# Performance work log

Hardware: AMD Instinct MI355X
Metric: run time of the kernel (lower is better)

Reference implementation:

```python
import jax, jax.numpy as jnp
import numpy as np

B, T, I = 8192, 20, 16
H1, H2, FC = 128, 64, 32


def _lstm(x_tbi, Wih, Whh, bih, bhh, H):
    """PyTorch-convention LSTM. x_tbi: (T,B,in). Gate order: i,f,g,o. Returns (T,B,H) hidden seq."""
    Tn, Bn = x_tbi.shape[0], x_tbi.shape[1]
    # precompute input projection for all timesteps: (T,B,4H)
    xz = jnp.einsum('tbi,gi->tbg', x_tbi, Wih) + (bih + bhh)

    def step(carry, xz_t):
        h, c = carry
        z = xz_t + h @ Whh.T  # (B,4H)
        i = jax.nn.sigmoid(z[:, 0*H:1*H])
        f = jax.nn.sigmoid(z[:, 1*H:2*H])
        g = jnp.tanh(z[:, 2*H:3*H])
        o = jax.nn.sigmoid(z[:, 3*H:4*H])
        c = f * c + i * g
        h = o * jnp.tanh(c)
        return (h, c), h

    h0 = jnp.zeros((Bn, H), x_tbi.dtype)
    c0 = jnp.zeros((Bn, H), x_tbi.dtype)
    _, hs = jax.lax.scan(step, (h0, c0), xz)
    return hs  # (T,B,H)


def setup_inputs() -> dict:
    key = jax.random.key(0)
    ks = jax.random.split(key, 16)
    s1 = 1.0 / np.sqrt(H1)
    s2 = 1.0 / np.sqrt(H2)
    u = lambda k, shape, s: jax.random.uniform(k, shape, jnp.float32, -s, s)
    return {
        'x': jax.random.normal(ks[0], (B, T, I), jnp.float32),
        'Wih1': u(ks[1], (4 * H1, I), s1),
        'Whh1': u(ks[2], (4 * H1, H1), s1),
        'bih1': u(ks[3], (4 * H1,), s1),
        'bhh1': u(ks[4], (4 * H1,), s1),
        'Wih2': u(ks[5], (4 * H2, H1), s2),
        'Whh2': u(ks[6], (4 * H2, H2), s2),
        'bih2': u(ks[7], (4 * H2,), s2),
        'bhh2': u(ks[8], (4 * H2,), s2),
        'gamma': jnp.ones((H2,), jnp.float32),
        'beta': jnp.zeros((H2,), jnp.float32),
        'W1': u(ks[9], (FC, H2), 1.0 / np.sqrt(H2)),
        'b1': u(ks[10], (FC,), 1.0 / np.sqrt(H2)),
        'W2': u(ks[11], (1, FC), 1.0 / np.sqrt(FC)),
        'b2': u(ks[12], (1,), 1.0 / np.sqrt(FC)),
    }


def reference(x, Wih1, Whh1, bih1, bhh1, Wih2, Whh2, bih2, bhh2, gamma, beta, W1, b1, W2, b2):
    # dropout layers are identity (eval mode)
    x_tbi = jnp.transpose(x, (1, 0, 2))           # (T,B,I)
    out1 = _lstm(x_tbi, Wih1, Whh1, bih1, bhh1, H1)  # (T,B,H1)
    out2 = _lstm(out1, Wih2, Whh2, bih2, bhh2, H2)   # (T,B,H2)
    last = out2[-1]                               # (B,H2)
    # LayerNorm over H2
    mu = jnp.mean(last, axis=-1, keepdims=True)
    var = jnp.mean((last - mu) ** 2, axis=-1, keepdims=True)
    normed = (last - mu) * jax.lax.rsqrt(var + 1e-5) * gamma + beta
    h = jax.nn.relu(normed @ W1.T + b1)           # (B,FC)
    logit = h @ W2.T + b2                         # (B,1)
    return logit[:, 0]
```

## Files before the change

kernel.cpp:

```cpp
#include <hip/hip_runtime.h>

#define TS 20
#define BATCH 8192
#define LOG2E 1.4426950408889634f

typedef _Float16 half8 __attribute__((ext_vector_type(8)));
typedef float f32x4 __attribute__((ext_vector_type(4)));

__device__ __forceinline__ float fexp2(float x) {
#if __has_builtin(__builtin_amdgcn_exp2f)
    return __builtin_amdgcn_exp2f(x);
#else
    return exp2f(x);
#endif
}
__device__ __forceinline__ float sig2(float zp)  { return __builtin_amdgcn_rcpf(1.0f + fexp2(-zp)); }
__device__ __forceinline__ float tanh2(float zp) { return 1.0f - 2.0f * __builtin_amdgcn_rcpf(1.0f + fexp2(zp)); }
__device__ __forceinline__ int swz(int r) { return (r & 7) ^ (((r >> 3) & 1) << 2); }

extern "C" __global__ __launch_bounds__(512, 1)
void fused_lstm_kernel(const float* __restrict__ x,
                       const float* __restrict__ Wih1, const float* __restrict__ Whh1,
                       const float* __restrict__ bih1, const float* __restrict__ bhh1,
                       const float* __restrict__ Wih2, const float* __restrict__ Whh2,
                       const float* __restrict__ bih2, const float* __restrict__ bhh2,
                       const float* __restrict__ gamma, const float* __restrict__ beta,
                       const float* __restrict__ W1fc, const float* __restrict__ b1fc,
                       const float* __restrict__ W2fc, const float* __restrict__ b2fc,
                       float* __restrict__ out)
{
    __shared__ __align__(16) _Float16 bf2l[4 * 4 * 6 * 64 * 8];
    __shared__ __align__(16) _Float16 Hb[2][2][16][128];
    __shared__ __align__(16) _Float16 Hc[2][2][16][72];
    __shared__ __align__(16) _Float16 Xb[32][328];
    __shared__ float h2f[32][68];

    const int tid  = threadIdx.x;
    const int lane = tid & 63;
    const int w    = tid >> 6;
    const int lrow = lane & 15;
    const int lgrp = lane >> 4;
    const int b0   = blockIdx.x * 32;

    half8 bf[4][5];
    float bias1[4];
#pragma unroll
    for (int g = 0; g < 4; ++g) {
        const float sc = (g == 2) ? 2.0f * LOG2E : LOG2E;
        const int n = g * 128 + w * 16 + lrow;
        bias1[g] = (bih1[n] + bhh1[n]) * sc;
#pragma unroll
        for (int ch = 0; ch < 5; ++ch) {
            half8 v;
            if (ch < 4) {
                const float4 p0 = *(const float4*)&Whh1[n * 128 + ch * 32 + lgrp * 8];
                const float4 p1 = *(const float4*)&Whh1[n * 128 + ch * 32 + lgrp * 8 + 4];
                v[0]=(_Float16)(p0.x*sc); v[1]=(_Float16)(p0.y*sc); v[2]=(_Float16)(p0.z*sc); v[3]=(_Float16)(p0.w*sc);
                v[4]=(_Float16)(p1.x*sc); v[5]=(_Float16)(p1.y*sc); v[6]=(_Float16)(p1.z*sc); v[7]=(_Float16)(p1.w*sc);
            } else if (lgrp < 2) {
                const float4 p0 = *(const float4*)&Wih1[n * 16 + lgrp * 8];
                const float4 p1 = *(const float4*)&Wih1[n * 16 + lgrp * 8 + 4];
                v[0]=(_Float16)(p0.x*sc); v[1]=(_Float16)(p0.y*sc); v[2]=(_Float16)(p0.z*sc); v[3]=(_Float16)(p0.w*sc);
                v[4]=(_Float16)(p1.x*sc); v[5]=(_Float16)(p1.y*sc); v[6]=(_Float16)(p1.z*sc); v[7]=(_Float16)(p1.w*sc);
            } else {
#pragma unroll
                for (int j = 0; j < 8; ++j) v[j] = (_Float16)0.0f;
            }
            bf[g][ch] = v;
        }
    }

    const int cg = w & 3;
    const int mt = w >> 2;
    float bias2[4];
#pragma unroll
    for (int g = 0; g < 4; ++g) {
        const float sc = (g == 2) ? 2.0f * LOG2E : LOG2E;
        const int n = g * 64 + cg * 16 + lrow;
        bias2[g] = (bih2[n] + bhh2[n]) * sc;
    }
    if (w < 4) {
#pragma unroll
        for (int g = 0; g < 4; ++g) {
            const float sc = (g == 2) ? 2.0f * LOG2E : LOG2E;
            const int n = g * 64 + w * 16 + lrow;
#pragma unroll
            for (int ch = 0; ch < 6; ++ch) {
                const float4 p0 = (ch < 4) ? *(const float4*)&Wih2[n * 128 + ch * 32 + lgrp * 8]
                                           : *(const float4*)&Whh2[n * 64 + (ch - 4) * 32 + lgrp * 8];
                const float4 p1 = (ch < 4) ? *(const float4*)&Wih2[n * 128 + ch * 32 + lgrp * 8 + 4]
                                           : *(const float4*)&Whh2[n * 64 + (ch - 4) * 32 + lgrp * 8 + 4];
                half8 v;
                v[0]=(_Float16)(p0.x*sc); v[1]=(_Float16)(p0.y*sc); v[2]=(_Float16)(p0.z*sc); v[3]=(_Float16)(p0.w*sc);
                v[4]=(_Float16)(p1.x*sc); v[5]=(_Float16)(p1.y*sc); v[6]=(_Float16)(p1.z*sc); v[7]=(_Float16)(p1.w*sc);
                ((half8*)bf2l)[((w * 4 + g) * 6 + ch) * 64 + lane] = v;
            }
        }
    }

    for (int i = tid; i < 2 * 2 * 16 * 128; i += 512) (&Hb[0][0][0][0])[i] = (_Float16)0.0f;
    for (int i = tid; i < 2 * 2 * 16 * 72;  i += 512) (&Hc[0][0][0][0])[i] = (_Float16)0.0f;
    for (int i = tid; i < 32 * 320; i += 512) {
        const int r = i / 320, k = i % 320;
        Xb[r][k] = (_Float16)x[(size_t)(b0 + r) * 320 + k];
    }
    half8 kzero;
#pragma unroll
    for (int j = 0; j < 8; ++j) kzero[j] = (_Float16)0.0f;

    float c1[2][4] = {{0.f,0.f,0.f,0.f},{0.f,0.f,0.f,0.f}};
    float c2[4] = {0.f, 0.f, 0.f, 0.f};
    const int hu  = (w << 1) | (lrow >> 3);
    const int hlo = lrow & 7;
    const int szr = swz(lrow);
    const int cell2 = (cg << 4) | lrow;

    __syncthreads();

    for (int t = 0; t < TS; ++t) {
        const int s = t & 1;
        f32x4 z[2][4];
#pragma unroll
        for (int tile = 0; tile < 2; ++tile)
#pragma unroll
            for (int g = 0; g < 4; ++g) z[tile][g] = (f32x4){bias1[g], bias1[g], bias1[g], bias1[g]};
#pragma unroll
        for (int ch = 0; ch < 5; ++ch) {
#pragma unroll
            for (int tile = 0; tile < 2; ++tile) {
                half8 a;
                if (ch < 4) a = *(const half8*)&Hb[s ^ 1][tile][lrow][(((ch << 2) | lgrp) ^ szr) * 8];
                else        a = (lgrp < 2) ? *(const half8*)&Xb[tile * 16 + lrow][t * 16 + lgrp * 8] : kzero;
#pragma unroll
                for (int g = 0; g < 4; ++g)
                    z[tile][g] = __builtin_amdgcn_mfma_f32_16x16x32_f16(a, bf[g][ch], z[tile][g], 0, 0, 0);
            }
        }
#pragma unroll
        for (int tile = 0; tile < 2; ++tile)
#pragma unroll
            for (int j = 0; j < 4; ++j) {
                const float iv = sig2 (z[tile][0][j]);
                const float fv = sig2 (z[tile][1][j]);
                const float gv = tanh2(z[tile][2][j]);
                const float ov = sig2 (z[tile][3][j]);
                const float cn = fv * c1[tile][j] + iv * gv;
                c1[tile][j] = cn;
                const float h = ov * tanh2(2.0f * LOG2E * cn);
                const int m = (lgrp << 2) | j;
                Hb[s][tile][m][((hu ^ swz(m)) << 3) | hlo] = (_Float16)h;
            }
        __syncthreads();
        {
            half8 a2[6];
#pragma unroll
            for (int ch = 0; ch < 4; ++ch)
                a2[ch] = *(const half8*)&Hb[s][mt][lrow][(((ch << 2) | lgrp) ^ szr) * 8];
#pragma unroll
            for (int ch = 4; ch < 6; ++ch)
                a2[ch] = *(const half8*)&Hc[s ^ 1][mt][lrow][(ch - 4) * 32 + lgrp * 8];
            f32x4 z2[4];
#pragma unroll
            for (int g = 0; g < 4; ++g) {
                f32x4 acc = {bias2[g], bias2[g], bias2[g], bias2[g]};
#pragma unroll
                for (int ch = 0; ch < 6; ++ch) {
                    const half8 bfrag = ((const half8*)bf2l)[((cg * 4 + g) * 6 + ch) * 64 + lane];
                    acc = __builtin_amdgcn_mfma_f32_16x16x32_f16(a2[ch], bfrag, acc, 0, 0, 0);
                }
                z2[g] = acc;
            }
#pragma unroll
            for (int j = 0; j < 4; ++j) {
                const float iv = sig2 (z2[0][j]);
                const float fv = sig2 (z2[1][j]);
                const float gv = tanh2(z2[2][j]);
                const float ov = sig2 (z2[3][j]);
                const float cn = fv * c2[j] + iv * gv;
                c2[j] = cn;
                const float h = ov * tanh2(2.0f * LOG2E * cn);
                const int m = (lgrp << 2) | j;
                Hc[s][mt][m][cell2] = (_Float16)h;
                if (t == TS - 1) h2f[(mt << 4) | m][cell2] = h;
            }
        }
    }
    __syncthreads();

    {
        const int m = tid >> 4, q = tid & 15;
        const float v0 = h2f[m][q * 4 + 0];
        const float v1 = h2f[m][q * 4 + 1];
        const float v2 = h2f[m][q * 4 + 2];
        const float v3 = h2f[m][q * 4 + 3];
        float ssum = v0 + v1 + v2 + v3;
        ssum += __shfl_xor(ssum, 1); ssum += __shfl_xor(ssum, 2);
        ssum += __shfl_xor(ssum, 4); ssum += __shfl_xor(ssum, 8);
        const float mean = ssum * (1.0f / 64.0f);
        const float d0 = v0 - mean, d1 = v1 - mean, d2 = v2 - mean, d3 = v3 - mean;
        float vs = d0 * d0 + d1 * d1 + d2 * d2 + d3 * d3;
        vs += __shfl_xor(vs, 1); vs += __shfl_xor(vs, 2);
        vs += __shfl_xor(vs, 4); vs += __shfl_xor(vs, 8);
        const float rstd = rsqrtf(vs * (1.0f / 64.0f) + 1e-5f);
        const int i0 = q * 4;
        h2f[m][i0 + 0] = d0 * rstd * gamma[i0 + 0] + beta[i0 + 0];
        h2f[m][i0 + 1] = d1 * rstd * gamma[i0 + 1] + beta[i0 + 1];
        h2f[m][i0 + 2] = d2 * rstd * gamma[i0 + 2] + beta[i0 + 2];
        h2f[m][i0 + 3] = d3 * rstd * gamma[i0 + 3] + beta[i0 + 3];
    }
    __syncthreads();
    {
        const int o = tid & 31;
        const int mgrp = tid >> 5;
#pragma unroll
        for (int rr = 0; rr < 2; ++rr) {
            const int m = mgrp + rr * 16;
            float acc = b1fc[o];
#pragma unroll 8
            for (int k = 0; k < 64; ++k) acc += h2f[m][k] * W1fc[o * 64 + k];
            const float hv = fmaxf(acc, 0.0f);
            float p = hv * W2fc[o];
            p += __shfl_xor(p, 1); p += __shfl_xor(p, 2);
            p += __shfl_xor(p, 4); p += __shfl_xor(p, 8); p += __shfl_xor(p, 16);
            if (o == 0) out[b0 + m] = p + b2fc[0];
        }
    }
}

extern "C" void kernel_launch(void* const* d_in, const int* in_sizes, int n_in,
                              void* d_out, int out_size, void* d_ws, size_t ws_size,
                              hipStream_t stream) {
    (void)in_sizes; (void)n_in; (void)d_ws; (void)ws_size; (void)out_size;
    const float* x_p    = (const float*)d_in[0];
    const float* Wih1_p = (const float*)d_in[1];
    const float* Whh1_p = (const float*)d_in[2];
    const float* bih1_p = (const float*)d_in[3];
    const float* bhh1_p = (const float*)d_in[4];
    const float* Wih2_p = (const float*)d_in[5];
    const float* Whh2_p = (const float*)d_in[6];
    const float* bih2_p = (const float*)d_in[7];
    const float* bhh2_p = (const float*)d_in[8];
    const float* gamma_p = (const float*)d_in[9];
    const float* beta_p  = (const float*)d_in[10];
    const float* W1_p   = (const float*)d_in[11];
    const float* b1_p   = (const float*)d_in[12];
    const float* W2_p   = (const float*)d_in[13];
    const float* b2_p   = (const float*)d_in[14];
    float* out_p = (float*)d_out;

    fused_lstm_kernel<<<dim3(BATCH / 32), dim3(512), 0, stream>>>(
        x_p, Wih1_p, Whh1_p, bih1_p, bhh1_p,
        Wih2_p, Whh2_p, bih2_p, bhh2_p,
        gamma_p, beta_p, W1_p, b1_p, W2_p, b2_p, out_p);
}
```

Measured before the change: 77.85 us.

## Halve block to 256 threads and skew layer-2 one step behind layer-1

The block shrinks from 8 to 4 waves. Each wave now computes two layer-1 column groups, keeping their weights in registers, and both batch tiles of layer 2. Layer 2 for step t-1 runs inside the same barrier interval as layer 1 for step t, with a final drain step after the loop, so one __syncthreads per timestep is removed. The aim is fewer barriers and possibly two blocks per CU given the relaxed launch bounds. In exchange each wave does twice the MFMA work per step and register pressure rises (40 half8 weight fragments), which may cut occupancy or cause spills.

```diff
diff --git a/kernel.cpp b/kernel.cpp
--- a/kernel.cpp
+++ b/kernel.cpp
@@ -18,16 +18,16 @@
 __device__ __forceinline__ float tanh2(float zp) { return 1.0f - 2.0f * __builtin_amdgcn_rcpf(1.0f + fexp2(zp)); }
 __device__ __forceinline__ int swz(int r) { return (r & 7) ^ (((r >> 3) & 1) << 2); }
 
-extern "C" __global__ __launch_bounds__(512, 1)
-void fused_lstm_kernel(const float* __restrict__ x,
-                       const float* __restrict__ Wih1, const float* __restrict__ Whh1,
-                       const float* __restrict__ bih1, const float* __restrict__ bhh1,
-                       const float* __restrict__ Wih2, const float* __restrict__ Whh2,
-                       const float* __restrict__ bih2, const float* __restrict__ bhh2,
-                       const float* __restrict__ gamma, const float* __restrict__ beta,
-                       const float* __restrict__ W1fc, const float* __restrict__ b1fc,
-                       const float* __restrict__ W2fc, const float* __restrict__ b2fc,
-                       float* __restrict__ out)
+extern "C" __global__ __launch_bounds__(256)
+void fused_lstm_fat_kernel(const float* __restrict__ x,
+                           const float* __restrict__ Wih1, const float* __restrict__ Whh1,
+                           const float* __restrict__ bih1, const float* __restrict__ bhh1,
+                           const float* __restrict__ Wih2, const float* __restrict__ Whh2,
+                           const float* __restrict__ bih2, const float* __restrict__ bhh2,
+                           const float* __restrict__ gamma, const float* __restrict__ beta,
+                           const float* __restrict__ W1fc, const float* __restrict__ b1fc,
+                           const float* __restrict__ W2fc, const float* __restrict__ b2fc,
+                           float* __restrict__ out)
 {
     __shared__ __align__(16) _Float16 bf2l[4 * 4 * 6 * 64 * 8];
     __shared__ __align__(16) _Float16 Hb[2][2][16][128];
@@ -42,65 +42,59 @@
     const int lgrp = lane >> 4;
     const int b0   = blockIdx.x * 32;
 
-    half8 bf[4][5];
-    float bias1[4];
+    half8 bf1[2][4][5];
+    float bias1[2][4];
+#pragma unroll
+    for (int cgi = 0; cgi < 2; ++cgi) {
+        const int cg = w + cgi * 4;
+#pragma unroll
+        for (int g = 0; g < 4; ++g) {
+            const float sc = (g == 2) ? 2.0f * LOG2E : LOG2E;
+            const int n = g * 128 + cg * 16 + lrow;
+            bias1[cgi][g] = (bih1[n] + bhh1[n]) * sc;
+#pragma unroll
+            for (int ch = 0; ch < 5; ++ch) {
+                half8 v;
+                if (ch < 4) {
+                    const float4 p0 = *(const float4*)&Whh1[n * 128 + ch * 32 + lgrp * 8];
+                    const float4 p1 = *(const float4*)&Whh1[n * 128 + ch * 32 + lgrp * 8 + 4];
+                    v[0]=(_Float16)(p0.x*sc); v[1]=(_Float16)(p0.y*sc); v[2]=(_Float16)(p0.z*sc); v[3]=(_Float16)(p0.w*sc);
+                    v[4]=(_Float16)(p1.x*sc); v[5]=(_Float16)(p1.y*sc); v[6]=(_Float16)(p1.z*sc); v[7]=(_Float16)(p1.w*sc);
+                } else if (lgrp < 2) {
+                    const float4 p0 = *(const float4*)&Wih1[n * 16 + lgrp * 8];
+                    const float4 p1 = *(const float4*)&Wih1[n * 16 + lgrp * 8 + 4];
+                    v[0]=(_Float16)(p0.x*sc); v[1]=(_Float16)(p0.y*sc); v[2]=(_Float16)(p0.z*sc); v[3]=(_Float16)(p0.w*sc);
+                    v[4]=(_Float16)(p1.x*sc); v[5]=(_Float16)(p1.y*sc); v[6]=(_Float16)(p1.z*sc); v[7]=(_Float16)(p1.w*sc);
+                } else {
+#pragma unroll
+                    for (int j = 0; j < 8; ++j) v[j] = (_Float16)0.0f;
+                }
+                bf1[cgi][g][ch] = v;
+            }
+        }
+    }
+    float bias2[4];
 #pragma unroll
     for (int g = 0; g < 4; ++g) {
         const float sc = (g == 2) ? 2.0f * LOG2E : LOG2E;
-        const int n = g * 128 + w * 16 + lrow;
-        bias1[g] = (bih1[n] + bhh1[n]) * sc;
-#pragma unroll
-        for (int ch = 0; ch < 5; ++ch) {
+        const int n = g * 64 + w * 16 + lrow;
+        bias2[g] = (bih2[n] + bhh2[n]) * sc;
+#pragma unroll
+        for (int ch = 0; ch < 6; ++ch) {
+            const float4 p0 = (ch < 4) ? *(const float4*)&Wih2[n * 128 + ch * 32 + lgrp * 8]
+                                       : *(const float4*)&Whh2[n * 64 + (ch - 4) * 32 + lgrp * 8];
+            const float4 p1 = (ch < 4) ? *(const float4*)&Wih2[n * 128 + ch * 32 + lgrp * 8 + 4]
+                                       : *(const float4*)&Whh2[n * 64 + (ch - 4) * 32 + lgrp * 8 + 4];
             half8 v;
-            if (ch < 4) {
-                const float4 p0 = *(const float4*)&Whh1[n * 128 + ch * 32 + lgrp * 8];
-                const float4 p1 = *(const float4*)&Whh1[n * 128 + ch * 32 + lgrp * 8 + 4];
-                v[0]=(_Float16)(p0.x*sc); v[1]=(_Float16)(p0.y*sc); v[2]=(_Float16)(p0.z*sc); v[3]=(_Float16)(p0.w*sc);
-                v[4]=(_Float16)(p1.x*sc); v[5]=(_Float16)(p1.y*sc); v[6]=(_Float16)(p1.z*sc); v[7]=(_Float16)(p1.w*sc);
-            } else if (lgrp < 2) {
-                const float4 p0 = *(const float4*)&Wih1[n * 16 + lgrp * 8];
-                const float4 p1 = *(const float4*)&Wih1[n * 16 + lgrp * 8 + 4];
-                v[0]=(_Float16)(p0.x*sc); v[1]=(_Float16)(p0.y*sc); v[2]=(_Float16)(p0.z*sc); v[3]=(_Float16)(p0.w*sc);
-                v[4]=(_Float16)(p1.x*sc); v[5]=(_Float16)(p1.y*sc); v[6]=(_Float16)(p1.z*sc); v[7]=(_Float16)(p1.w*sc);
-            } else {
-#pragma unroll
-                for (int j = 0; j < 8; ++j) v[j] = (_Float16)0.0f;
-            }
-            bf[g][ch] = v;
-        }
-    }
-
-    const int cg = w & 3;
-    const int mt = w >> 2;
-    float bias2[4];
-#pragma unroll
-    for (int g = 0; g < 4; ++g) {
-        const float sc = (g == 2) ? 2.0f * LOG2E : LOG2E;
-        const int n = g * 64 + cg * 16 + lrow;
-        bias2[g] = (bih2[n] + bhh2[n]) * sc;
-    }
-    if (w < 4) {
-#pragma unroll
-        for (int g = 0; g < 4; ++g) {
-            const float sc = (g == 2) ? 2.0f * LOG2E : LOG2E;
-            const int n = g * 64 + w * 16 + lrow;
-#pragma unroll
-            for (int ch = 0; ch < 6; ++ch) {
-                const float4 p0 = (ch < 4) ? *(const float4*)&Wih2[n * 128 + ch * 32 + lgrp * 8]
-                                           : *(const float4*)&Whh2[n * 64 + (ch - 4) * 32 + lgrp * 8];
-                const float4 p1 = (ch < 4) ? *(const float4*)&Wih2[n * 128 + ch * 32 + lgrp * 8 + 4]
-                                           : *(const float4*)&Whh2[n * 64 + (ch - 4) * 32 + lgrp * 8 + 4];
-                half8 v;
-                v[0]=(_Float16)(p0.x*sc); v[1]=(_Float16)(p0.y*sc); v[2]=(_Float16)(p0.z*sc); v[3]=(_Float16)(p0.w*sc);
-                v[4]=(_Float16)(p1.x*sc); v[5]=(_Float16)(p1.y*sc); v[6]=(_Float16)(p1.z*sc); v[7]=(_Float16)(p1.w*sc);
-                ((half8*)bf2l)[((w * 4 + g) * 6 + ch) * 64 + lane] = v;
-            }
-        }
-    }
-
-    for (int i = tid; i < 2 * 2 * 16 * 128; i += 512) (&Hb[0][0][0][0])[i] = (_Float16)0.0f;
-    for (int i = tid; i < 2 * 2 * 16 * 72;  i += 512) (&Hc[0][0][0][0])[i] = (_Float16)0.0f;
-    for (int i = tid; i < 32 * 320; i += 512) {
+            v[0]=(_Float16)(p0.x*sc); v[1]=(_Float16)(p0.y*sc); v[2]=(_Float16)(p0.z*sc); v[3]=(_Float16)(p0.w*sc);
+            v[4]=(_Float16)(p1.x*sc); v[5]=(_Float16)(p1.y*sc); v[6]=(_Float16)(p1.z*sc); v[7]=(_Float16)(p1.w*sc);
+            ((half8*)bf2l)[((w * 4 + g) * 6 + ch) * 64 + lane] = v;
+        }
+    }
+
+    for (int i = tid; i < 2 * 2 * 16 * 128; i += 256) (&Hb[0][0][0][0])[i] = (_Float16)0.0f;
+    for (int i = tid; i < 2 * 2 * 16 * 72;  i += 256) (&Hc[0][0][0][0])[i] = (_Float16)0.0f;
+    for (int i = tid; i < 32 * 320; i += 256) {
         const int r = i / 320, k = i % 320;
         Xb[r][k] = (_Float16)x[(size_t)(b0 + r) * 320 + k];
     }
@@ -108,67 +102,106 @@
 #pragma unroll
     for (int j = 0; j < 8; ++j) kzero[j] = (_Float16)0.0f;
 
-    float c1[2][4] = {{0.f,0.f,0.f,0.f},{0.f,0.f,0.f,0.f}};
-    float c2[4] = {0.f, 0.f, 0.f, 0.f};
-    const int hu  = (w << 1) | (lrow >> 3);
-    const int hlo = lrow & 7;
-    const int szr = swz(lrow);
-    const int cell2 = (cg << 4) | lrow;
+    float c1[2][2][4];
+    float c2[2][4];
+#pragma unroll
+    for (int a = 0; a < 2; ++a)
+#pragma unroll
+        for (int b = 0; b < 2; ++b)
+#pragma unroll
+            for (int j = 0; j < 4; ++j) { c1[a][b][j] = 0.f; if (b == 0) c2[a][j] = 0.f; }
+
+    const int szr   = swz(lrow);
+    const int hlo   = lrow & 7;
+    const int cell2 = (w << 4) | lrow;
 
     __syncthreads();
 
     for (int t = 0; t < TS; ++t) {
         const int s = t & 1;
-        f32x4 z[2][4];
-#pragma unroll
-        for (int tile = 0; tile < 2; ++tile)
-#pragma unroll
-            for (int g = 0; g < 4; ++g) z[tile][g] = (f32x4){bias1[g], bias1[g], bias1[g], bias1[g]};
-#pragma unroll
-        for (int ch = 0; ch < 5; ++ch) {
+        if (t > 0) {
+            const int sp = s ^ 1;
 #pragma unroll
             for (int tile = 0; tile < 2; ++tile) {
-                half8 a;
-                if (ch < 4) a = *(const half8*)&Hb[s ^ 1][tile][lrow][(((ch << 2) | lgrp) ^ szr) * 8];
-                else        a = (lgrp < 2) ? *(const half8*)&Xb[tile * 16 + lrow][t * 16 + lgrp * 8] : kzero;
-#pragma unroll
-                for (int g = 0; g < 4; ++g)
-                    z[tile][g] = __builtin_amdgcn_mfma_f32_16x16x32_f16(a, bf[g][ch], z[tile][g], 0, 0, 0);
-            }
-        }
-#pragma unroll
-        for (int tile = 0; tile < 2; ++tile)
-#pragma unroll
-            for (int j = 0; j < 4; ++j) {
-                const float iv = sig2 (z[tile][0][j]);
-                const float fv = sig2 (z[tile][1][j]);
-                const float gv = tanh2(z[tile][2][j]);
-                const float ov = sig2 (z[tile][3][j]);
-                const float cn = fv * c1[tile][j] + iv * gv;
-                c1[tile][j] = cn;
-                const float h = ov * tanh2(2.0f * LOG2E * cn);
-                const int m = (lgrp << 2) | j;
-                Hb[s][tile][m][((hu ^ swz(m)) << 3) | hlo] = (_Float16)h;
-            }
+                f32x4 z2[4];
+#pragma unroll
+                for (int g = 0; g < 4; ++g) z2[g] = (f32x4){bias2[g], bias2[g], bias2[g], bias2[g]};
+#pragma unroll
+                for (int ch = 0; ch < 6; ++ch) {
+                    const half8 a2 = (ch < 4)
+                        ? *(const half8*)&Hb[sp][tile][lrow][(((ch << 2) | lgrp) ^ szr) * 8]
+                        : *(const half8*)&Hc[sp ^ 1][tile][lrow][(ch - 4) * 32 + lgrp * 8];
+#pragma unroll
+                    for (int g = 0; g < 4; ++g) {
+                        const half8 wf = ((const half8*)bf2l)[((w * 4 + g) * 6 + ch) * 64 + lane];
+                        z2[g] = __builtin_amdgcn_mfma_f32_16x16x32_f16(a2, wf, z2[g], 0, 0, 0);
+                    }
+                }
+#pragma unroll
+                for (int j = 0; j < 4; ++j) {
+                    const float iv = sig2 (z2[0][j]);
+                    const float fv = sig2 (z2[1][j]);
+                    const float gv = tanh2(z2[2][j]);
+                    const float ov = sig2 (z2[3][j]);
+                    const float cn = fv * c2[tile][j] + iv * gv;
+                    c2[tile][j] = cn;
+                    const float h = ov * tanh2(2.0f * LOG2E * cn);
+                    const int m = (lgrp << 2) | j;
+                    Hc[sp][tile][m][cell2] = (_Float16)h;
+                }
+            }
+        }
+#pragma unroll
+        for (int tile = 0; tile < 2; ++tile) {
+#pragma unroll
+            for (int cgi = 0; cgi < 2; ++cgi) {
+                f32x4 z[4];
+#pragma unroll
+                for (int g = 0; g < 4; ++g) z[g] = (f32x4){bias1[cgi][g], bias1[cgi][g], bias1[cgi][g], bias1[cgi][g]};
+#pragma unroll
+                for (int ch = 0; ch < 5; ++ch) {
+                    half8 a;
+                    if (ch < 4) a = *(const half8*)&Hb[s ^ 1][tile][lrow][(((ch << 2) | lgrp) ^ szr) * 8];
+                    else        a = (lgrp < 2) ? *(const half8*)&Xb[tile * 16 + lrow][t * 16 + lgrp * 8] : kzero;
+#pragma unroll
+                    for (int g = 0; g < 4; ++g)
+                        z[g] = __builtin_amdgcn_mfma_f32_16x16x32_f16(a, bf1[cgi][g][ch], z[g], 0, 0, 0);
+                }
+                const int cg = w + cgi * 4;
+                const int hu = (cg << 1) | (lrow >> 3);
+#pragma unroll
+                for (int j = 0; j < 4; ++j) {
+                    const float iv = sig2 (z[0][j]);
+                    const float fv = sig2 (z[1][j]);
+                    const float gv = tanh2(z[2][j]);
+                    const float ov = sig2 (z[3][j]);
+                    const float cn = fv * c1[tile][cgi][j] + iv * gv;
+                    c1[tile][cgi][j] = cn;
+                    const float h = ov * tanh2(2.0f * LOG2E * cn);
+                    const int m = (lgrp << 2) | j;
+                    Hb[s][tile][m][((hu ^ swz(m)) << 3) | hlo] = (_Float16)h;
+                }
+            }
+        }
         __syncthreads();
-        {
-            half8 a2[6];
-#pragma unroll
-            for (int ch = 0; ch < 4; ++ch)
-                a2[ch] = *(const half8*)&Hb[s][mt][lrow][(((ch << 2) | lgrp) ^ szr) * 8];
-#pragma unroll
-            for (int ch = 4; ch < 6; ++ch)
-                a2[ch] = *(const half8*)&Hc[s ^ 1][mt][lrow][(ch - 4) * 32 + lgrp * 8];
+    }
+    {
+        const int sp = (TS - 1) & 1;
+#pragma unroll
+        for (int tile = 0; tile < 2; ++tile) {
             f32x4 z2[4];
 #pragma unroll
-            for (int g = 0; g < 4; ++g) {
-                f32x4 acc = {bias2[g], bias2[g], bias2[g], bias2[g]};
-#pragma unroll
-                for (int ch = 0; ch < 6; ++ch) {
-                    const half8 bfrag = ((const half8*)bf2l)[((cg * 4 + g) * 6 + ch) * 64 + lane];
-                    acc = __builtin_amdgcn_mfma_f32_16x16x32_f16(a2[ch], bfrag, acc, 0, 0, 0);
-                }
-                z2[g] = acc;
+            for (int g = 0; g < 4; ++g) z2[g] = (f32x4){bias2[g], bias2[g], bias2[g], bias2[g]};
+#pragma unroll
+            for (int ch = 0; ch < 6; ++ch) {
+                const half8 a2 = (ch < 4)
+                    ? *(const half8*)&Hb[sp][tile][lrow][(((ch << 2) | lgrp) ^ szr) * 8]
+                    : *(const half8*)&Hc[sp ^ 1][tile][lrow][(ch - 4) * 32 + lgrp * 8];
+#pragma unroll
+                for (int g = 0; g < 4; ++g) {
+                    const half8 wf = ((const half8*)bf2l)[((w * 4 + g) * 6 + ch) * 64 + lane];
+                    z2[g] = __builtin_amdgcn_mfma_f32_16x16x32_f16(a2, wf, z2[g], 0, 0, 0);
+                }
             }
 #pragma unroll
             for (int j = 0; j < 4; ++j) {
@@ -176,45 +209,44 @@
                 const float fv = sig2 (z2[1][j]);
                 const float gv = tanh2(z2[2][j]);
                 const float ov = sig2 (z2[3][j]);
-                const float cn = fv * c2[j] + iv * gv;
-                c2[j] = cn;
+                const float cn = fv * c2[tile][j] + iv * gv;
+                c2[tile][j] = cn;
                 const float h = ov * tanh2(2.0f * LOG2E * cn);
                 const int m = (lgrp << 2) | j;
-                Hc[s][mt][m][cell2] = (_Float16)h;
-                if (t == TS - 1) h2f[(mt << 4) | m][cell2] = h;
+                h2f[(tile << 4) | m][cell2] = h;
             }
         }
     }
     __syncthreads();
 
     {
-        const int m = tid >> 4, q = tid & 15;
-        const float v0 = h2f[m][q * 4 + 0];
-        const float v1 = h2f[m][q * 4 + 1];
-        const float v2 = h2f[m][q * 4 + 2];
-        const float v3 = h2f[m][q * 4 + 3];
-        float ssum = v0 + v1 + v2 + v3;
-        ssum += __shfl_xor(ssum, 1); ssum += __shfl_xor(ssum, 2);
-        ssum += __shfl_xor(ssum, 4); ssum += __shfl_xor(ssum, 8);
+        const int m = tid >> 3, q = tid & 7;
+        float v[8];
+#pragma unroll
+        for (int i = 0; i < 8; ++i) v[i] = h2f[m][q * 8 + i];
+        float ssum = 0.f;
+#pragma unroll
+        for (int i = 0; i < 8; ++i) ssum += v[i];
+        ssum += __shfl_xor(ssum, 1); ssum += __shfl_xor(ssum, 2); ssum += __shfl_xor(ssum, 4);
         const float mean = ssum * (1.0f / 64.0f);
-        const float d0 = v0 - mean, d1 = v1 - mean, d2 = v2 - mean, d3 = v3 - mean;
-        float vs = d0 * d0 + d1 * d1 + d2 * d2 + d3 * d3;
-        vs += __shfl_xor(vs, 1); vs += __shfl_xor(vs, 2);
-        vs += __shfl_xor(vs, 4); vs += __shfl_xor(vs, 8);
+        float vs = 0.f;
+#pragma unroll
+        for (int i = 0; i < 8; ++i) { const float d = v[i] - mean; vs += d * d; }
+        vs += __shfl_xor(vs, 1); vs += __shfl_xor(vs, 2); vs += __shfl_xor(vs, 4);
         const float rstd = rsqrtf(vs * (1.0f / 64.0f) + 1e-5f);
-        const int i0 = q * 4;
-        h2f[m][i0 + 0] = d0 * rstd * gamma[i0 + 0] + beta[i0 + 0];
-        h2f[m][i0 + 1] = d1 * rstd * gamma[i0 + 1] + beta[i0 + 1];
-        h2f[m][i0 + 2] = d2 * rstd * gamma[i0 + 2] + beta[i0 + 2];
-        h2f[m][i0 + 3] = d3 * rstd * gamma[i0 + 3] + beta[i0 + 3];
+#pragma unroll
+        for (int i = 0; i < 8; ++i) {
+            const int k = q * 8 + i;
+            h2f[m][k] = (v[i] - mean) * rstd * gamma[k] + beta[k];
+        }
     }
     __syncthreads();
     {
-        const int o = tid & 31;
-        const int mgrp = tid >> 5;
-#pragma unroll
-        for (int rr = 0; rr < 2; ++rr) {
-            const int m = mgrp + rr * 16;
+        const int o  = tid & 31;
+        const int mg = tid >> 5;
+#pragma unroll
+        for (int rr = 0; rr < 4; ++rr) {
+            const int m = mg + rr * 8;
             float acc = b1fc[o];
 #pragma unroll 8
             for (int k = 0; k < 64; ++k) acc += h2f[m][k] * W1fc[o * 64 + k];
@@ -248,7 +280,7 @@
     const float* b2_p   = (const float*)d_in[14];
     float* out_p = (float*)d_out;
 
-    fused_lstm_kernel<<<dim3(BATCH / 32), dim3(512), 0, stream>>>(
+    fused_lstm_fat_kernel<<<dim3(BATCH / 32), dim3(256), 0, stream>>>(
         x_p, Wih1_p, Whh1_p, bih1_p, bhh1_p,
         Wih2_p, Whh2_p, bih2_p, bhh2_p,
         gamma_p, beta_p, W1_p, b1_p, W2_p, b2_p, out_p);
```

Result: slower. 110.0 us (+41.3%).

## Skew LSTM layer pipeline to overlap layer-2 step t with layer-1 step t+1

Applied to the files above, without the earlier changes.

Restructures the time loop so that layer-2 work for step t and layer-1 work for step t+1 run in the same barrier interval. This cuts the number of block-wide barriers per step from two to one and lets the two layers' MFMA and transcendental work interleave. Layer-1 MFMAs are regrouped per tile, and layer-2 operand loads move inside the chunk loop. The cost is higher register pressure from having both phases live, plus prologue and epilogue handling.

```diff
diff --git a/kernel.cpp b/kernel.cpp
--- a/kernel.cpp
+++ b/kernel.cpp
@@ -19,15 +19,15 @@
 __device__ __forceinline__ int swz(int r) { return (r & 7) ^ (((r >> 3) & 1) << 2); }
 
 extern "C" __global__ __launch_bounds__(512, 1)
-void fused_lstm_kernel(const float* __restrict__ x,
-                       const float* __restrict__ Wih1, const float* __restrict__ Whh1,
-                       const float* __restrict__ bih1, const float* __restrict__ bhh1,
-                       const float* __restrict__ Wih2, const float* __restrict__ Whh2,
-                       const float* __restrict__ bih2, const float* __restrict__ bhh2,
-                       const float* __restrict__ gamma, const float* __restrict__ beta,
-                       const float* __restrict__ W1fc, const float* __restrict__ b1fc,
-                       const float* __restrict__ W2fc, const float* __restrict__ b2fc,
-                       float* __restrict__ out)
+void fused_lstm_rot_kernel(const float* __restrict__ x,
+                           const float* __restrict__ Wih1, const float* __restrict__ Whh1,
+                           const float* __restrict__ bih1, const float* __restrict__ bhh1,
+                           const float* __restrict__ Wih2, const float* __restrict__ Whh2,
+                           const float* __restrict__ bih2, const float* __restrict__ bhh2,
+                           const float* __restrict__ gamma, const float* __restrict__ beta,
+                           const float* __restrict__ W1fc, const float* __restrict__ b1fc,
+                           const float* __restrict__ W2fc, const float* __restrict__ b2fc,
+                           float* __restrict__ out)
 {
     __shared__ __align__(16) _Float16 bf2l[4 * 4 * 6 * 64 * 8];
     __shared__ __align__(16) _Float16 Hb[2][2][16][128];
@@ -115,76 +115,79 @@
     const int szr = swz(lrow);
     const int cell2 = (cg << 4) | lrow;
 
-    __syncthreads();
-
-    for (int t = 0; t < TS; ++t) {
-        const int s = t & 1;
-        f32x4 z[2][4];
-#pragma unroll
-        for (int tile = 0; tile < 2; ++tile)
-#pragma unroll
-            for (int g = 0; g < 4; ++g) z[tile][g] = (f32x4){bias1[g], bias1[g], bias1[g], bias1[g]};
-#pragma unroll
-        for (int ch = 0; ch < 5; ++ch) {
-#pragma unroll
-            for (int tile = 0; tile < 2; ++tile) {
-                half8 a;
-                if (ch < 4) a = *(const half8*)&Hb[s ^ 1][tile][lrow][(((ch << 2) | lgrp) ^ szr) * 8];
-                else        a = (lgrp < 2) ? *(const half8*)&Xb[tile * 16 + lrow][t * 16 + lgrp * 8] : kzero;
+    auto phaseA = [&](int tt) {
+        const int sA = tt & 1;
+#pragma unroll
+        for (int tile = 0; tile < 2; ++tile) {
+            half8 a[5];
+#pragma unroll
+            for (int ch = 0; ch < 4; ++ch)
+                a[ch] = *(const half8*)&Hb[sA ^ 1][tile][lrow][(((ch << 2) | lgrp) ^ szr) * 8];
+            a[4] = (lgrp < 2) ? *(const half8*)&Xb[tile * 16 + lrow][tt * 16 + lgrp * 8] : kzero;
+            f32x4 z[4];
+#pragma unroll
+            for (int g = 0; g < 4; ++g) z[g] = (f32x4){bias1[g], bias1[g], bias1[g], bias1[g]};
+#pragma unroll
+            for (int ch = 0; ch < 5; ++ch)
 #pragma unroll
                 for (int g = 0; g < 4; ++g)
-                    z[tile][g] = __builtin_amdgcn_mfma_f32_16x16x32_f16(a, bf[g][ch], z[tile][g], 0, 0, 0);
-            }
-        }
-#pragma unroll
-        for (int tile = 0; tile < 2; ++tile)
+                    z[g] = __builtin_amdgcn_mfma_f32_16x16x32_f16(a[ch], bf[g][ch], z[g], 0, 0, 0);
 #pragma unroll
             for (int j = 0; j < 4; ++j) {
-                const float iv = sig2 (z[tile][0][j]);
-                const float fv = sig2 (z[tile][1][j]);
-                const float gv = tanh2(z[tile][2][j]);
-                const float ov = sig2 (z[tile][3][j]);
+                const float iv = sig2 (z[0][j]);
+                const float fv = sig2 (z[1][j]);
+                const float gv = tanh2(z[2][j]);
+                const float ov = sig2 (z[3][j]);
                 const float cn = fv * c1[tile][j] + iv * gv;
                 c1[tile][j] = cn;
                 const float h = ov * tanh2(2.0f * LOG2E * cn);
                 const int m = (lgrp << 2) | j;
-                Hb[s][tile][m][((hu ^ swz(m)) << 3) | hlo] = (_Float16)h;
-            }
+                Hb[sA][tile][m][((hu ^ swz(m)) << 3) | hlo] = (_Float16)h;
+            }
+        }
+    };
+    auto phaseB = [&](int tt, bool last) {
+        const int sB = tt & 1;
+        f32x4 z2[4];
+#pragma unroll
+        for (int g = 0; g < 4; ++g) z2[g] = (f32x4){bias2[g], bias2[g], bias2[g], bias2[g]};
+#pragma unroll
+        for (int ch = 0; ch < 6; ++ch) {
+            const half8 a2 = (ch < 4)
+                ? *(const half8*)&Hb[sB][mt][lrow][(((ch << 2) | lgrp) ^ szr) * 8]
+                : *(const half8*)&Hc[sB ^ 1][mt][lrow][(ch - 4) * 32 + lgrp * 8];
+#pragma unroll
+            for (int g = 0; g < 4; ++g) {
+                const half8 wf = ((const half8*)bf2l)[((cg * 4 + g) * 6 + ch) * 64 + lane];
+                z2[g] = __builtin_amdgcn_mfma_f32_16x16x32_f16(a2, wf, z2[g], 0, 0, 0);
+            }
+        }
+#pragma unroll
+        for (int j = 0; j < 4; ++j) {
+            const float iv = sig2 (z2[0][j]);
+            const float fv = sig2 (z2[1][j]);
+            const float gv = tanh2(z2[2][j]);
+            const float ov = sig2 (z2[3][j]);
+            const float cn = fv * c2[j] + iv * gv;
+            c2[j] = cn;
+            const float h = ov * tanh2(2.0f * LOG2E * cn);
+            const int m = (lgrp << 2) | j;
+            Hc[sB][mt][m][cell2] = (_Float16)h;
+            if (last) h2f[(mt << 4) | m][cell2] = h;
+        }
+    };
+
+    __syncthreads();
+    phaseA(0);
+    __syncthreads();
+
+#pragma unroll 2
+    for (int t = 0; t < TS - 1; ++t) {
+        phaseB(t, false);
+        phaseA(t + 1);
         __syncthreads();
-        {
-            half8 a2[6];
-#pragma unroll
-            for (int ch = 0; ch < 4; ++ch)
-                a2[ch] = *(const half8*)&Hb[s][mt][lrow][(((ch << 2) | lgrp) ^ szr) * 8];
-#pragma unroll
-            for (int ch = 4; ch < 6; ++ch)
-                a2[ch] = *(const half8*)&Hc[s ^ 1][mt][lrow][(ch - 4) * 32 + lgrp * 8];
-            f32x4 z2[4];
-#pragma unroll
-            for (int g = 0; g < 4; ++g) {
-                f32x4 acc = {bias2[g], bias2[g], bias2[g], bias2[g]};
-#pragma unroll
-                for (int ch = 0; ch < 6; ++ch) {
-                    const half8 bfrag = ((const half8*)bf2l)[((cg * 4 + g) * 6 + ch) * 64 + lane];
-                    acc = __builtin_amdgcn_mfma_f32_16x16x32_f16(a2[ch], bfrag, acc, 0, 0, 0);
-                }
-                z2[g] = acc;
-            }
-#pragma unroll
-            for (int j = 0; j < 4; ++j) {
-                const float iv = sig2 (z2[0][j]);
-                const float fv = sig2 (z2[1][j]);
-                const float gv = tanh2(z2[2][j]);
-                const float ov = sig2 (z2[3][j]);
-                const float cn = fv * c2[j] + iv * gv;
-                c2[j] = cn;
-                const float h = ov * tanh2(2.0f * LOG2E * cn);
-                const int m = (lgrp << 2) | j;
-                Hc[s][mt][m][cell2] = (_Float16)h;
-                if (t == TS - 1) h2f[(mt << 4) | m][cell2] = h;
-            }
-        }
-    }
+    }
+    phaseB(TS - 1, true);
     __syncthreads();
 
     {
@@ -248,7 +251,7 @@
     const float* b2_p   = (const float*)d_in[14];
     float* out_p = (float*)d_out;
 
-    fused_lstm_kernel<<<dim3(BATCH / 32), dim3(512), 0, stream>>>(
+    fused_lstm_rot_kernel<<<dim3(BATCH / 32), dim3(512), 0, stream>>>(
         x_p, Wih1_p, Whh1_p, bih1_p, bhh1_p,
         Wih2_p, Whh2_p, bih2_p, bhh2_p,
         gamma_p, beta_p, W1_p, b1_p, W2_p, b2_p, out_p);
```

After: 76.88 us. No clear change (-1.2%).
